# Optimization experiments

Hardware: AMD Instinct MI355X
Metric: run time of the kernel (lower is better)

Reference implementation:

```python
import jax, jax.numpy as jnp
import numpy as np

N_HEAD = 16


def setup_inputs() -> dict:
    key = jax.random.key(0)
    k1, k2, k3 = jax.random.split(key, 3)
    B, T, C = 2, 2048, 1024
    x = jax.random.normal(k1, (B, T, C), dtype=jnp.float32)
    # stored as [in, out] so projection is x @ w (equiv. to torch Linear with W=[out,in])
    w_attn = jax.random.normal(k2, (C, 3 * C), dtype=jnp.float32) * 0.02
    w_proj = jax.random.normal(k3, (C, C), dtype=jnp.float32) * 0.02
    return {"x": x, "w_attn": w_attn, "w_proj": w_proj}


def reference(x, w_attn, w_proj):
    B, T, C = x.shape
    H = N_HEAD
    D = C // H
    qkv = x @ w_attn                                  # [B,T,3C]
    q, k, v = jnp.split(qkv, 3, axis=-1)
    q = q.reshape(B, T, H, D).transpose(0, 2, 1, 3)   # [B,H,T,D]
    k = k.reshape(B, T, H, D).transpose(0, 2, 1, 3)
    v = v.reshape(B, T, H, D).transpose(0, 2, 1, 3)
    scale = 1.0 / jnp.sqrt(jnp.asarray(D, dtype=x.dtype))
    att = jnp.einsum("bhqd,bhkd->bhqk", q, k) * scale  # [B,H,T,T]
    causal = jnp.tril(jnp.ones((T, T), dtype=bool))
    att = jnp.where(causal[None, None], att, jnp.finfo(att.dtype).min)
    att = jax.nn.softmax(att, axis=-1)                 # dropout p=0 (eval)
    y = jnp.einsum("bhqk,bhkd->bhqd", att, v)          # [B,H,T,D]
    y = y.transpose(0, 2, 1, 3).reshape(B, T, C)
    return y @ w_proj
```

## Files before the change

kernel.cpp:

```cpp
#include <hip/hip_runtime.h>
#include <hip/hip_bf16.h>

using u16 = unsigned short;
using u32 = unsigned int;

typedef __attribute__((ext_vector_type(8))) short s16x8;
typedef __attribute__((ext_vector_type(4))) short s16x4;
typedef __attribute__((ext_vector_type(8))) __bf16 bf16x8;
typedef __attribute__((ext_vector_type(4))) float f32x4;
typedef __attribute__((ext_vector_type(2))) unsigned u32x2;

static __device__ __forceinline__ u16 f2bf(float f) {
  u32 u = __builtin_bit_cast(u32, f);
  u32 r = u + 0x7FFFu + ((u >> 16) & 1u);
  return (u16)(r >> 16);
}

static __device__ __forceinline__ u32 pk2bf(float lo, float hi) {
  __hip_bfloat162 h = __float22bfloat162_rn(make_float2(lo, hi));
  u32 r;
  __builtin_memcpy(&r, &h, 4);
  return r;
}

static __device__ __forceinline__ f32x4 mfma16(s16x8 a, s16x8 b, f32x4 c) {
  return __builtin_amdgcn_mfma_f32_16x16x32_bf16(
      __builtin_bit_cast(bf16x8, a), __builtin_bit_cast(bf16x8, b), c, 0, 0, 0);
}

#define GLOAD_LDS16(gp, lp)                                                    \
  __builtin_amdgcn_global_load_lds(                                            \
      (const __attribute__((address_space(1))) void*)(gp),                     \
      (__attribute__((address_space(3))) void*)(lp), 16, 0, 0)

__global__ __launch_bounds__(256) void k_cvt(const float* __restrict__ in,
                                             u16* __restrict__ out, int n) {
  int i = (blockIdx.x * 256 + threadIdx.x) * 8;
  if (i >= n) return;
  const float4 v0 = *(const float4*)(in + i);
  const float4 v1 = *(const float4*)(in + i + 4);
  s16x8 o;
  o[0] = f2bf(v0.x); o[1] = f2bf(v0.y); o[2] = f2bf(v0.z); o[3] = f2bf(v0.w);
  o[4] = f2bf(v1.x); o[5] = f2bf(v1.y); o[6] = f2bf(v1.z); o[7] = f2bf(v1.w);
  *(s16x8*)(out + i) = o;
}

__global__ __launch_bounds__(256) void k_transpose_cvt(const float* __restrict__ src,
                                                       u16* __restrict__ dst,
                                                       int K, int N) {
  __shared__ float tile[64][65];
  const int n0 = blockIdx.x * 64, k0 = blockIdx.y * 64;
  const int c = threadIdx.x & 63, r4 = threadIdx.x >> 6;
#pragma unroll
  for (int i = 0; i < 16; ++i) {
    int r = (i << 2) + r4;
    tile[r][c] = src[(k0 + r) * N + n0 + c];
  }
  __syncthreads();
#pragma unroll
  for (int i = 0; i < 16; ++i) {
    int r = (i << 2) + r4;
    dst[(n0 + r) * K + k0 + c] = f2bf(tile[c][r]);
  }
}

template <int MODE>
__global__ __launch_bounds__(256) void k_gemm(
    const u16* __restrict__ A, const u16* __restrict__ BT,
    u16* __restrict__ qg, u16* __restrict__ kg, u16* __restrict__ vtg,
    float* __restrict__ cout, int M, int N, int K) {
  __shared__ __align__(16) u16 As[128 * 32];
  __shared__ __align__(16) u16 Bs[128 * 32];
  __shared__ __align__(16) u16 Ct[(MODE == 0) ? (128 * 132) : 8];
  const int t = threadIdx.x;
  const int lane = t & 63;
  const int w = t >> 6, wr = w >> 1, wc = w & 1;
  const int lrow = lane & 15, lkg = lane >> 4;
  const int m0 = blockIdx.y * 128, n0 = blockIdx.x * 128;

  const int ch1 = t + 256;
  const int ra0 = t >> 2, ca0 = (t & 3) << 3;
  const int ra1 = ch1 >> 2, ca1 = (ch1 & 3) << 3;
  const u16* gA0 = A + (m0 + ra0) * K + ca0;
  const u16* gA1 = A + (m0 + ra1) * K + ca1;
  const u16* gB0 = BT + (n0 + ra0) * K + ca0;
  const u16* gB1 = BT + (n0 + ra1) * K + ca1;
  u16* lA0 = &As[t * 8];
  u16* lA1 = &As[ch1 * 8];
  u16* lB0 = &Bs[t * 8];
  u16* lB1 = &Bs[ch1 * 8];

  f32x4 acc[4][4];
#pragma unroll
  for (int m = 0; m < 4; ++m)
#pragma unroll
    for (int n = 0; n < 4; ++n) acc[m][n] = (f32x4){0.f, 0.f, 0.f, 0.f};

  for (int k0 = 0; k0 < K; k0 += 32) {
    GLOAD_LDS16(gA0 + k0, lA0);
    GLOAD_LDS16(gA1 + k0, lA1);
    GLOAD_LDS16(gB0 + k0, lB0);
    GLOAD_LDS16(gB1 + k0, lB1);
    __syncthreads();
    s16x8 af[4], bfr[4];
#pragma unroll
    for (int m = 0; m < 4; ++m)
      af[m] = *(const s16x8*)&As[(wr * 64 + m * 16 + lrow) * 32 + lkg * 8];
#pragma unroll
    for (int n = 0; n < 4; ++n)
      bfr[n] = *(const s16x8*)&Bs[(wc * 64 + n * 16 + lrow) * 32 + lkg * 8];
#pragma unroll
    for (int m = 0; m < 4; ++m)
#pragma unroll
      for (int n = 0; n < 4; ++n) acc[m][n] = mfma16(af[m], bfr[n], acc[m][n]);
    __syncthreads();
  }

  if (MODE == 0) {
    const int part = n0 >> 10;
    const int b = m0 >> 11;
    const int tt0 = m0 & 2047;
    if (part < 2) {
#pragma unroll
      for (int m = 0; m < 4; ++m)
#pragma unroll
        for (int n = 0; n < 4; ++n)
#pragma unroll
          for (int r = 0; r < 4; ++r) {
            const int tl = wr * 64 + m * 16 + lkg * 4 + r;
            const int rem = (n0 & 1023) + wc * 64 + n * 16 + lrow;
            const int h = rem >> 6, d = rem & 63;
            const int bh = b * 16 + h;
            const float v = acc[m][n][r];
            if (part == 0)
              qg[(bh * 2048 + tt0 + tl) * 64 + d] = f2bf(v * 0.18033688f);
            else
              kg[(bh * 2048 + tt0 + tl) * 64 + d] = f2bf(v);
          }
    } else {
#pragma unroll
      for (int m = 0; m < 4; ++m)
#pragma unroll
        for (int n = 0; n < 4; ++n) {
          const int cl2 = wc * 64 + n * 16 + lrow;
          const int tl = wr * 64 + m * 16 + lkg * 4;
          s16x4 pk;
#pragma unroll
          for (int r = 0; r < 4; ++r) pk[r] = f2bf(acc[m][n][r]);
          *(s16x4*)&Ct[cl2 * 132 + tl] = pk;
        }
      __syncthreads();
      const long vrow0 = (long)b * 1024 + (n0 & 1023);
      const int cl = t >> 1;
      const int ch = (t & 1) << 6;
      const u16* csrc = &Ct[cl * 132 + ch];
      u16* vdst = vtg + (vrow0 + cl) * 2048 + tt0 + ch;
#pragma unroll
      for (int j = 0; j < 8; ++j) {
        const s16x4 a4 = *(const s16x4*)&csrc[j * 8];
        const s16x4 b4 = *(const s16x4*)&csrc[j * 8 + 4];
        s16x8 v8;
        v8[0] = a4[0]; v8[1] = a4[1]; v8[2] = a4[2]; v8[3] = a4[3];
        v8[4] = b4[0]; v8[5] = b4[1]; v8[6] = b4[2]; v8[7] = b4[3];
        *(s16x8*)&vdst[j * 8] = v8;
      }
    }
  } else {
#pragma unroll
    for (int m = 0; m < 4; ++m)
#pragma unroll
      for (int n = 0; n < 4; ++n)
#pragma unroll
        for (int r = 0; r < 4; ++r) {
          const int rg = m0 + wr * 64 + m * 16 + lkg * 4 + r;
          const int cg = n0 + wc * 64 + n * 16 + lrow;
          cout[rg * N + cg] = acc[m][n][r];
        }
  }
}

__global__ __launch_bounds__(256) void k_gemm2(const u16* __restrict__ A,
                                               const u16* __restrict__ BT,
                                               float* __restrict__ cout, int M,
                                               int N, int K) {
  __shared__ __align__(16) u16 As[64 * 32];
  __shared__ __align__(16) u16 Bs[128 * 32];
  const int t = threadIdx.x;
  const int lane = t & 63;
  const int w = t >> 6, wr = w >> 1, wc = w & 1;
  const int lrow = lane & 15, lkg = lane >> 4;
  const int m0 = blockIdx.y * 64, n0 = blockIdx.x * 128;

  const int ra = t >> 2, ca = (t & 3) << 3;
  const u16* gA = A + (m0 + ra) * K + ca;
  const u16* gB0 = BT + (n0 + ra) * K + ca;
  const u16* gB1 = BT + (n0 + 64 + ra) * K + ca;
  u16* lA = &As[t * 8];
  u16* lB0 = &Bs[t * 8];
  u16* lB1 = &Bs[(t + 256) * 8];

  f32x4 acc[2][4];
#pragma unroll
  for (int m = 0; m < 2; ++m)
#pragma unroll
    for (int n = 0; n < 4; ++n) acc[m][n] = (f32x4){0.f, 0.f, 0.f, 0.f};

  for (int k0 = 0; k0 < K; k0 += 32) {
    GLOAD_LDS16(gA + k0, lA);
    GLOAD_LDS16(gB0 + k0, lB0);
    GLOAD_LDS16(gB1 + k0, lB1);
    __syncthreads();
    s16x8 af[2], bfr[4];
#pragma unroll
    for (int m = 0; m < 2; ++m)
      af[m] = *(const s16x8*)&As[(wr * 32 + m * 16 + lrow) * 32 + lkg * 8];
#pragma unroll
    for (int n = 0; n < 4; ++n)
      bfr[n] = *(const s16x8*)&Bs[(wc * 64 + n * 16 + lrow) * 32 + lkg * 8];
#pragma unroll
    for (int m = 0; m < 2; ++m)
#pragma unroll
      for (int n = 0; n < 4; ++n) acc[m][n] = mfma16(af[m], bfr[n], acc[m][n]);
    __syncthreads();
  }

#pragma unroll
  for (int m = 0; m < 2; ++m)
#pragma unroll
    for (int n = 0; n < 4; ++n)
#pragma unroll
      for (int r = 0; r < 4; ++r) {
        const int rg = m0 + wr * 32 + m * 16 + lkg * 4 + r;
        const int cg = n0 + wc * 64 + n * 16 + lrow;
        cout[rg * N + cg] = acc[m][n][r];
      }
}

__global__ __launch_bounds__(256) void k_attn(const u16* __restrict__ qg,
                                              const u16* __restrict__ kg,
                                              const u16* __restrict__ vtg,
                                              u16* __restrict__ yb) {
  __shared__ __align__(16) u16 Ks[2][64 * 64];
  __shared__ __align__(16) u16 Vs[2][64 * 64];
  __shared__ __align__(16) u16 Ps[4][32 * 72];
  const int t = threadIdx.x;
  const int lane = t & 63, w = t >> 6;
  const int lrow = lane & 15, lkg = lane >> 4;
  const int bx = blockIdx.x, by = blockIdx.y;
  const int qs = (by & 16) ? (15 - bx) : bx;
  const int bh = by;
  const int qw0 = qs * 128 + w * 32;
  const int hb = bh & 15, bb = bh >> 4;
  const int sw = lrow & 7;
  const f32x4 z4 = {0.f, 0.f, 0.f, 0.f};
  const s16x8 ones8 = {0x3F80, 0x3F80, 0x3F80, 0x3F80,
                       0x3F80, 0x3F80, 0x3F80, 0x3F80};

  const u16* kbase = kg + ((long)bh << 11) * 64;
  const u16* vbase = vtg + ((long)bh << 6) * 2048;

  const int srow = lane >> 3;
  const int sxor8 = ((lane & 7) ^ srow) << 3;

  s16x8 aq[2][2];
#pragma unroll
  for (int m = 0; m < 2; ++m)
#pragma unroll
    for (int kk = 0; kk < 2; ++kk)
      aq[m][kk] = *(const s16x8*)&qg[((bh << 11) + qw0 + m * 16 + lrow) * 64 +
                                     kk * 32 + lkg * 8];

  f32x4 o[2][4];
  f32x4 os[2];
  float mst[2];
#pragma unroll
  for (int m = 0; m < 2; ++m) {
#pragma unroll
    for (int d = 0; d < 4; ++d) o[m][d] = z4;
    os[m] = z4;
    mst[m] = -3e38f;
  }

  const int nt = 2 * qs + 2;

#define STAGE(BUF, TT)                                                         \
  {                                                                            \
    const int kv0s = (TT) << 6;                                                \
    _Pragma("unroll") for (int i = 0; i < 2; ++i) {                            \
      const int rr = ((i * 4 + w) << 3) + srow;                                \
      const int dst = (((i * 4 + w) << 6) + lane) << 3;                        \
      GLOAD_LDS16(kbase + ((kv0s + rr) << 6) + sxor8, &Ks[BUF][dst]);          \
      GLOAD_LDS16(vbase + ((long)rr << 11) + kv0s + sxor8, &Vs[BUF][dst]);     \
    }                                                                          \
  }

  STAGE(0, 0);
  int buf = 0;
  for (int tt = 0; tt < nt; ++tt) {
    const int kv0 = tt << 6;
    if (tt + 1 < nt) {
      STAGE(buf ^ 1, tt + 1);
      asm volatile("s_waitcnt vmcnt(4)" ::: "memory");
    } else {
      asm volatile("s_waitcnt vmcnt(0)" ::: "memory");
    }
    __builtin_amdgcn_s_barrier();
    __builtin_amdgcn_sched_barrier(0);

    if (kv0 < qw0 + 32) {
      f32x4 s[2][4];
      __builtin_amdgcn_s_setprio(1);
#pragma unroll
      for (int c = 0; c < 4; ++c) {
        const int krow = c * 16 + lrow;
        s16x8 bk0 = *(const s16x8*)&Ks[buf][krow * 64 + ((lkg ^ sw) << 3)];
        s16x8 bk1 = *(const s16x8*)&Ks[buf][krow * 64 + (((4 + lkg) ^ sw) << 3)];
#pragma unroll
        for (int m = 0; m < 2; ++m)
          s[m][c] = mfma16(bk1, aq[m][1], mfma16(bk0, aq[m][0], z4));
      }
      __builtin_amdgcn_s_setprio(0);

      if (kv0 + 64 > qw0) {
#pragma unroll
        for (int m = 0; m < 2; ++m) {
          const int qrow = qw0 + m * 16 + lrow;
#pragma unroll
          for (int c = 0; c < 4; ++c) {
            const int kvb = kv0 + c * 16 + lkg * 4;
#pragma unroll
            for (int r = 0; r < 4; ++r)
              if (kvb + r > qrow) s[m][c][r] = -3e38f;
          }
        }
      }

      u16* PW = Ps[w];
#pragma unroll
      for (int m = 0; m < 2; ++m) {
        float lm = s[m][0][0];
#pragma unroll
        for (int c = 0; c < 4; ++c)
#pragma unroll
          for (int r = 0; r < 4; ++r) lm = fmaxf(lm, s[m][c][r]);
        lm = fmaxf(lm, __shfl_xor(lm, 16));
        lm = fmaxf(lm, __shfl_xor(lm, 32));
        const float mn = fmaxf(mst[m], lm);
        const float alm = exp2f(mst[m] - mn);
        mst[m] = mn;
#pragma unroll
        for (int d = 0; d < 4; ++d) o[m][d] *= alm;
        os[m] *= alm;
#pragma unroll
        for (int c = 0; c < 4; ++c) {
          const float p0 = exp2f(s[m][c][0] - mn);
          const float p1 = exp2f(s[m][c][1] - mn);
          const float p2 = exp2f(s[m][c][2] - mn);
          const float p3 = exp2f(s[m][c][3] - mn);
          const s16x4 pk4 =
              __builtin_bit_cast(s16x4, (u32x2){pk2bf(p0, p1), pk2bf(p2, p3)});
          *(s16x4*)&PW[(m * 16 + lrow) * 72 + c * 16 + lkg * 4] = pk4;
        }
      }

      s16x8 pb[2][2];
#pragma unroll
      for (int m = 0; m < 2; ++m)
#pragma unroll
        for (int kk = 0; kk < 2; ++kk)
          pb[m][kk] =
              *(const s16x8*)&PW[(m * 16 + lrow) * 72 + kk * 32 + lkg * 8];

      __builtin_amdgcn_s_setprio(1);
#pragma unroll
      for (int d = 0; d < 4; ++d) {
        const int vrow = d * 16 + lrow;
        s16x8 bv0 = *(const s16x8*)&Vs[buf][vrow * 64 + ((lkg ^ sw) << 3)];
        s16x8 bv1 = *(const s16x8*)&Vs[buf][vrow * 64 + (((4 + lkg) ^ sw) << 3)];
#pragma unroll
        for (int m = 0; m < 2; ++m)
          o[m][d] = mfma16(bv1, pb[m][1], mfma16(bv0, pb[m][0], o[m][d]));
      }
#pragma unroll
      for (int m = 0; m < 2; ++m)
        os[m] = mfma16(ones8, pb[m][1], mfma16(ones8, pb[m][0], os[m]));
      __builtin_amdgcn_s_setprio(0);
    }

    __builtin_amdgcn_s_barrier();
    buf ^= 1;
  }

#pragma unroll
  for (int m = 0; m < 2; ++m) {
    const float inv = 1.0f / os[m][0];
    const int q = qw0 + m * 16 + lrow;
    u16* yrow = yb + ((long)((bb << 11) + q)) * 1024 + hb * 64;
#pragma unroll
    for (int d = 0; d < 4; ++d) {
      const s16x4 pk4 = __builtin_bit_cast(
          s16x4, (u32x2){pk2bf(o[m][d][0] * inv, o[m][d][1] * inv),
                         pk2bf(o[m][d][2] * inv, o[m][d][3] * inv)});
      *(s16x4*)&yrow[d * 16 + lkg * 4] = pk4;
    }
  }
#undef STAGE
}

extern "C" void kernel_launch(void* const* d_in, const int* in_sizes, int n_in,
                              void* d_out, int out_size, void* d_ws,
                              size_t ws_size, hipStream_t stream) {
  const float* x = (const float*)d_in[0];
  const float* wa = (const float*)d_in[1];
  const float* wp = (const float*)d_in[2];
  float* out = (float*)d_out;
  u16* ws = (u16*)d_ws;

  u16* xb = ws;
  u16* wat = xb + 4194304;
  u16* wpt = wat + 3145728;
  u16* qg = wpt + 1048576;
  u16* kg = qg + 4194304;
  u16* vtg = kg + 4194304;
  u16* yb = vtg + 4194304;

  k_cvt<<<2048, 256, 0, stream>>>(x, xb, 4194304);
  k_transpose_cvt<<<dim3(48, 16), 256, 0, stream>>>(wa, wat, 1024, 3072);
  k_transpose_cvt<<<dim3(16, 16), 256, 0, stream>>>(wp, wpt, 1024, 1024);
  k_gemm<0><<<dim3(24, 32), 256, 0, stream>>>(xb, wat, qg, kg, vtg, nullptr,
                                              4096, 3072, 1024);
  k_attn<<<dim3(16, 32), 256, 0, stream>>>(qg, kg, vtg, yb);
  k_gemm2<<<dim3(8, 64), 256, 0, stream>>>(yb, wpt, out, 4096, 1024, 1024);
}
```

Before: 214.8 us.

## Split causal attention KV range into two partial blocks with combine kernel

The attention kernel now splits each query tile's KV range into two halves handled by separate blocks, doubling the grid from 512 to 1024 blocks. Each half writes an unnormalized bf16 output plus its running max and sum, and a new combine kernel merges the halves with log-sum-exp rescaling before writing y. This targets the under-filled, imbalanced 512-block launch across the GPU's compute units. In exchange it adds an extra kernel launch, extra global traffic for the partial outputs, and rounds the unnormalized partials to bf16.

```diff
diff --git a/kernel.cpp b/kernel.cpp
--- a/kernel.cpp
+++ b/kernel.cpp
@@ -14,6 +14,11 @@
   u32 u = __builtin_bit_cast(u32, f);
   u32 r = u + 0x7FFFu + ((u >> 16) & 1u);
   return (u16)(r >> 16);
+}
+
+static __device__ __forceinline__ float bf2f(u16 b) {
+  u32 u = ((u32)b) << 16;
+  return __builtin_bit_cast(float, u);
 }
 
 static __device__ __forceinline__ u32 pk2bf(float lo, float hi) {
@@ -236,10 +241,10 @@
       }
 }
 
-__global__ __launch_bounds__(256) void k_attn(const u16* __restrict__ qg,
-                                              const u16* __restrict__ kg,
-                                              const u16* __restrict__ vtg,
-                                              u16* __restrict__ yb) {
+__global__ __launch_bounds__(256) void k_attn_part(
+    const u16* __restrict__ qg, const u16* __restrict__ kg,
+    const u16* __restrict__ vtg, u16* __restrict__ Om,
+    float* __restrict__ ms, float* __restrict__ osv) {
   __shared__ __align__(16) u16 Ks[2][64 * 64];
   __shared__ __align__(16) u16 Vs[2][64 * 64];
   __shared__ __align__(16) u16 Ps[4][32 * 72];
@@ -247,10 +252,11 @@
   const int lane = t & 63, w = t >> 6;
   const int lrow = lane & 15, lkg = lane >> 4;
   const int bx = blockIdx.x, by = blockIdx.y;
-  const int qs = (by & 16) ? (15 - bx) : bx;
+  const int hsplit = bx >> 4;
+  const int qr = bx & 15;
+  const int qs = (by & 16) ? (15 - qr) : qr;
   const int bh = by;
   const int qw0 = qs * 128 + w * 32;
-  const int hb = bh & 15, bb = bh >> 4;
   const int sw = lrow & 7;
   const f32x4 z4 = {0.f, 0.f, 0.f, 0.f};
   const s16x8 ones8 = {0x3F80, 0x3F80, 0x3F80, 0x3F80,
@@ -281,7 +287,8 @@
     mst[m] = -3e38f;
   }
 
-  const int nt = 2 * qs + 2;
+  const int t0 = hsplit ? (qs + 1) : 0;
+  const int t1 = hsplit ? (2 * qs + 2) : (qs + 1);
 
 #define STAGE(BUF, TT)                                                         \
   {                                                                            \
@@ -294,11 +301,11 @@
     }                                                                          \
   }
 
-  STAGE(0, 0);
+  STAGE(0, t0);
   int buf = 0;
-  for (int tt = 0; tt < nt; ++tt) {
+  for (int tt = t0; tt < t1; ++tt) {
     const int kv0 = tt << 6;
-    if (tt + 1 < nt) {
+    if (tt + 1 < t1) {
       STAGE(buf ^ 1, tt + 1);
       asm volatile("s_waitcnt vmcnt(4)" ::: "memory");
     } else {
@@ -391,20 +398,50 @@
     buf ^= 1;
   }
 
+  const long rbase = ((long)(hsplit << 5) + bh) * 2048;
 #pragma unroll
   for (int m = 0; m < 2; ++m) {
-    const float inv = 1.0f / os[m][0];
     const int q = qw0 + m * 16 + lrow;
-    u16* yrow = yb + ((long)((bb << 11) + q)) * 1024 + hb * 64;
+    const long row = rbase + q;
+    u16* orow = Om + row * 64;
 #pragma unroll
     for (int d = 0; d < 4; ++d) {
       const s16x4 pk4 = __builtin_bit_cast(
-          s16x4, (u32x2){pk2bf(o[m][d][0] * inv, o[m][d][1] * inv),
-                         pk2bf(o[m][d][2] * inv, o[m][d][3] * inv)});
-      *(s16x4*)&yrow[d * 16 + lkg * 4] = pk4;
+          s16x4, (u32x2){pk2bf(o[m][d][0], o[m][d][1]),
+                         pk2bf(o[m][d][2], o[m][d][3])});
+      *(s16x4*)&orow[d * 16 + lkg * 4] = pk4;
     }
+    if (lkg == 0) {
+      ms[row] = mst[m];
+      osv[row] = os[m][0];
+    }
   }
 #undef STAGE
+}
+
+__global__ __launch_bounds__(256) void k_attn_comb(const u16* __restrict__ Om,
+                                                   const float* __restrict__ ms,
+                                                   const float* __restrict__ osv,
+                                                   u16* __restrict__ yb) {
+  const int gid = blockIdx.x * 256 + threadIdx.x;
+  const int row = gid >> 3;
+  const int d0 = (gid & 7) << 3;
+  const float mA = ms[row], mB = ms[65536 + row];
+  const float oA = osv[row], oB = osv[65536 + row];
+  const float M = fmaxf(mA, mB);
+  const float wA = exp2f(mA - M), wB = exp2f(mB - M);
+  const float inv = 1.0f / (wA * oA + wB * oB);
+  const float sA = wA * inv, sB = wB * inv;
+  const s16x8 a8 = *(const s16x8*)&Om[(long)row * 64 + d0];
+  const s16x8 b8 = *(const s16x8*)&Om[((long)row + 65536) * 64 + d0];
+  const int bh = row >> 11, q = row & 2047;
+  const int b = bh >> 4, hh = bh & 15;
+  u16* dst = yb + ((long)((b << 11) + q)) * 1024 + hh * 64 + d0;
+  s16x8 y8;
+#pragma unroll
+  for (int j = 0; j < 8; ++j)
+    y8[j] = f2bf(sA * bf2f((u16)a8[j]) + sB * bf2f((u16)b8[j]));
+  *(s16x8*)dst = y8;
 }
 
 extern "C" void kernel_launch(void* const* d_in, const int* in_sizes, int n_in,
@@ -423,12 +460,16 @@
   u16* kg = qg + 4194304;
   u16* vtg = kg + 4194304;
   u16* yb = vtg + 4194304;
+  u16* Om = yb + 4194304;
+  float* ms = (float*)(Om + 8388608);
+  float* osv = ms + 131072;
 
   k_cvt<<<2048, 256, 0, stream>>>(x, xb, 4194304);
   k_transpose_cvt<<<dim3(48, 16), 256, 0, stream>>>(wa, wat, 1024, 3072);
   k_transpose_cvt<<<dim3(16, 16), 256, 0, stream>>>(wp, wpt, 1024, 1024);
   k_gemm<0><<<dim3(24, 32), 256, 0, stream>>>(xb, wat, qg, kg, vtg, nullptr,
                                               4096, 3072, 1024);
-  k_attn<<<dim3(16, 32), 256, 0, stream>>>(qg, kg, vtg, yb);
+  k_attn_part<<<dim3(32, 32), 256, 0, stream>>>(qg, kg, vtg, Om, ms, osv);
+  k_attn_comb<<<2048, 256, 0, stream>>>(Om, ms, osv, yb);
   k_gemm2<<<dim3(8, 64), 256, 0, stream>>>(yb, wpt, out, 4096, 1024, 1024);
 }
```

Result: slower. 224.3 us (+4.4%).
